# Kernel optimization log

Measured on AMD Instinct MI355X. Metric: run time of the kernel, lower is better.

The kernel has to match this reference:

```python
import jax, jax.numpy as jnp
import numpy as np

B, N, DIM = 2, 2048, 1024
HEADS, DH = 16, 64
INNER = HEADS * DH
LN_EPS = 1e-5


def setup_inputs() -> dict:
    key = jax.random.key(0)
    ks = jax.random.split(key, 3)
    x = jax.random.normal(ks[0], (B, N, DIM), dtype=jnp.float32)
    ln_w = jnp.ones((DIM,), dtype=jnp.float32)
    ln_b = jnp.zeros((DIM,), dtype=jnp.float32)
    w_qkv = jax.random.normal(ks[1], (DIM, 3 * INNER), dtype=jnp.float32) * (DIM ** -0.5)
    w_out = jax.random.normal(ks[2], (INNER, DIM), dtype=jnp.float32) * (INNER ** -0.5)
    b_out = jnp.zeros((DIM,), dtype=jnp.float32)
    return {"x": x, "ln_w": ln_w, "ln_b": ln_b, "w_qkv": w_qkv, "w_out": w_out, "b_out": b_out}


def _rope(q, k):
    # q, k: (b, h, n, d) with d even; interleaved RoPE matching the torch module.
    n, d = q.shape[-2], q.shape[-1]
    inv_freq = jnp.exp(jnp.arange(0, d, 2, dtype=jnp.float32) * (-jnp.log(jnp.float32(10000.0)) / d))
    ang = jnp.arange(n, dtype=jnp.float32)[:, None] * inv_freq[None, :]  # (n, d/2)
    cos = jnp.repeat(jnp.cos(ang), 2, axis=-1)  # (n, d) -> broadcast over b,h
    sin = jnp.repeat(jnp.sin(ang), 2, axis=-1)

    def rot(t):
        t2 = t.reshape(*t.shape[:-1], d // 2, 2)  # pairs (even, odd)
        t2 = jnp.stack([-t2[..., 1], t2[..., 0]], axis=-1).reshape(t.shape)
        return t * cos + t2 * sin

    return rot(q), rot(k)


def reference(x, ln_w, ln_b, w_qkv, w_out, b_out):
    # LayerNorm
    mu = jnp.mean(x, axis=-1, keepdims=True)
    var = jnp.var(x, axis=-1, keepdims=True)
    xn = (x - mu) * jax.lax.rsqrt(var + LN_EPS) * ln_w + ln_b
    # QKV projection (no bias)
    qkv = xn @ w_qkv  # (b, n, 3*inner)
    q, k, v = jnp.split(qkv, 3, axis=-1)
    split_heads = lambda t: t.reshape(B, N, HEADS, DH).transpose(0, 2, 1, 3)  # b h n d
    q, k, v = split_heads(q), split_heads(k), split_heads(v)
    q, k = _rope(q, k)
    scale = DH ** -0.5
    dots = jnp.einsum('bhid,bhjd->bhij', q, k) * scale
    attn = jax.nn.softmax(dots, axis=-1)
    out = jnp.einsum('bhij,bhjd->bhid', attn, v)
    out = out.transpose(0, 2, 1, 3).reshape(B, N, INNER)  # b n (h d)
    return out @ w_out + b_out
```

## Files before the change

### kernel.cpp

```cpp
#include <hip/hip_runtime.h>

typedef unsigned short u16;
typedef unsigned int   u32;
typedef __bf16 bf16x8 __attribute__((ext_vector_type(8)));
typedef __bf16 bf16x2 __attribute__((ext_vector_type(2)));
typedef float  f32x4  __attribute__((ext_vector_type(4)));

#define B_     2
#define N_     2048
#define DIM_   1024
#define HEADS_ 16
#define DH_    64
#define BH_    (B_*HEADS_)
#define ROWS_  (B_*N_)

__device__ __forceinline__ u16 f2b(float f) {
  union { __bf16 h; u16 u; } v; v.h = (__bf16)f; return v.u;
}
__device__ __forceinline__ u32 pkb(float a, float b) {
  bf16x2 t; t[0] = (__bf16)a; t[1] = (__bf16)b;
  union { bf16x2 v; u32 u; } c; c.v = t; return c.u;
}
__device__ __forceinline__ float b2f(u16 h) {
  union { u32 u; float f; } v; v.u = ((u32)h) << 16;
  return v.f;
}
__device__ __forceinline__ void gload16(const void* g, void* l) {
  __builtin_amdgcn_global_load_lds(
      (const __attribute__((address_space(1))) void*)g,
      (__attribute__((address_space(3))) void*)l, 16, 0, 0);
}
__device__ __forceinline__ f32x4 mfma16(bf16x8 a, bf16x8 b, f32x4 c) {
  return __builtin_amdgcn_mfma_f32_16x16x32_bf16(a, b, c, 0, 0, 0);
}

__global__ __launch_bounds__(256) void prep_kernel(
    const float* __restrict__ x, const float* __restrict__ lw,
    const float* __restrict__ lb, const float* __restrict__ wqkv,
    const float* __restrict__ wout, u16* __restrict__ xn,
    u16* __restrict__ wqt, u16* __restrict__ wot) {
  __shared__ float tile[32][33];
  int blk = blockIdx.x, t = threadIdx.x;
  if (blk < 4096) {
    int r = blk;
    const float4* xr = (const float4*)(x + (size_t)r * DIM_);
    float4 v = xr[t];
    float s  = v.x + v.y + v.z + v.w;
    float s2 = v.x*v.x + v.y*v.y + v.z*v.z + v.w*v.w;
    #pragma unroll
    for (int off = 32; off >= 1; off >>= 1) {
      s  += __shfl_down(s, off);
      s2 += __shfl_down(s2, off);
    }
    int w = t >> 6, lane = t & 63;
    if (lane == 0) { tile[0][w] = s; tile[1][w] = s2; }
    __syncthreads();
    if (t == 0) {
      float S = tile[0][0]+tile[0][1]+tile[0][2]+tile[0][3];
      float S2 = tile[1][0]+tile[1][1]+tile[1][2]+tile[1][3];
      float mu = S * (1.0f/DIM_);
      float var = S2 * (1.0f/DIM_) - mu*mu;
      tile[2][0] = mu; tile[2][1] = rsqrtf(var + 1e-5f);
    }
    __syncthreads();
    float mu = tile[2][0], rs = tile[2][1];
    float4 wv = ((const float4*)lw)[t];
    float4 bv = ((const float4*)lb)[t];
    u32 lo = pkb((v.x-mu)*rs*wv.x + bv.x, (v.y-mu)*rs*wv.y + bv.y);
    u32 hi = pkb((v.z-mu)*rs*wv.z + bv.z, (v.w-mu)*rs*wv.w + bv.w);
    ((uint2*)xn)[(size_t)r*256 + t] = make_uint2(lo, hi);
  } else {
    const float* in; u16* outp; int R, C, c0, r0;
    if (blk < 7168) {
      int b2 = blk - 4096;
      in = wqkv; outp = wqt; R = 1024; C = 3072;
      c0 = (b2 % 96) * 32; r0 = (b2 / 96) * 32;
    } else {
      int b2 = blk - 7168;
      in = wout; outp = wot; R = 1024; C = 1024;
      c0 = (b2 & 31) * 32; r0 = (b2 >> 5) * 32;
    }
    int tx = t & 31, ty = t >> 5;
    #pragma unroll
    for (int i = 0; i < 4; i++)
      tile[ty + i*8][tx] = in[(size_t)(r0 + ty + i*8) * C + c0 + tx];
    __syncthreads();
    #pragma unroll
    for (int i = 0; i < 4; i++)
      outp[(size_t)(c0 + ty + i*8) * R + r0 + tx] = f2b(tile[tx][ty + i*8]);
  }
}

__global__ __launch_bounds__(256) void gemm_qkv(
    const u16* __restrict__ A, const u16* __restrict__ Bt,
    u16* __restrict__ qo, u16* __restrict__ ko, u16* __restrict__ vo) {
  const int K = 1024;
  __shared__ __align__(16) u16 lA[128*32];
  __shared__ __align__(16) u16 lB[128*32];
  int tid = threadIdx.x;
  int lane = tid & 63;
  int w = tid >> 6, wm = w >> 1, wn = w & 1;
  int l15 = lane & 15, g = lane >> 4;
  int bm = blockIdx.x, bn = blockIdx.y;
  const f32x4 z = {0.f, 0.f, 0.f, 0.f};
  f32x4 acc[4][4];
  #pragma unroll
  for (int i = 0; i < 4; i++)
    #pragma unroll
    for (int j = 0; j < 4; j++)
      acc[i][j] = z;
  const u16* ag = A  + (size_t)(bm*128 + (tid>>2)) * K + (tid&3)*8;
  const u16* bg = Bt + (size_t)(bn*128 + (tid>>2)) * K + (tid&3)*8;
  u16* la = lA + tid*8;
  u16* lb = lB + tid*8;
  for (int k0 = 0; k0 < K; k0 += 32) {
    gload16(ag + k0,                la);
    gload16(ag + (size_t)64*K + k0, la + 2048);
    gload16(bg + k0,                lb);
    gload16(bg + (size_t)64*K + k0, lb + 2048);
    __syncthreads();
    bf16x8 af[4], bfr[4];
    #pragma unroll
    for (int mt = 0; mt < 4; mt++)
      af[mt] = *(const bf16x8*)(lA + (wm*64 + mt*16 + l15)*32 + g*8);
    #pragma unroll
    for (int nt = 0; nt < 4; nt++)
      bfr[nt] = *(const bf16x8*)(lB + (wn*64 + nt*16 + l15)*32 + g*8);
    __builtin_amdgcn_s_setprio(1);
    #pragma unroll
    for (int mt = 0; mt < 4; mt++)
      #pragma unroll
      for (int nt = 0; nt < 4; nt++)
        acc[mt][nt] = mfma16(af[mt], bfr[nt], acc[mt][nt]);
    __builtin_amdgcn_s_setprio(0);
    __syncthreads();
  }
  #pragma unroll
  for (int mt = 0; mt < 4; mt++) {
    #pragma unroll
    for (int nt = 0; nt < 4; nt++) {
      #pragma unroll
      for (int reg = 0; reg < 4; reg++) {
        int rr = bm*128 + wm*64 + mt*16 + g*4 + reg;
        int cc = bn*128 + wn*64 + nt*16 + l15;
        float val = acc[mt][nt][reg];
        int which = cc >> 10, inner = cc & 1023;
        int h = inner >> 6, dd = inner & 63;
        int b = rr >> 11, np = rr & 2047;
        int bh = b*HEADS_ + h;
        if (which == 0)      qo[((size_t)(bh*2048 + np))*64 + dd] = f2b(val);
        else if (which == 1) ko[((size_t)(bh*2048 + np))*64 + dd] = f2b(val);
        else                 vo[((size_t)(bh*64 + dd))*2048 + np] = f2b(val);
      }
    }
  }
}

__global__ __launch_bounds__(256) void rope_k_kernel(u16* k) {
  int tid = blockIdx.x * 256 + threadIdx.x;
  int row = tid >> 3, sub = tid & 7;
  int n = row & 2047;
  u32* kp = (u32*)(k + (size_t)row * 64 + sub * 8);
  uint4 uk = *(uint4*)kp;
  float c4[4], s4[4];
  #pragma unroll
  for (int j = 0; j < 4; j++) {
    int p = sub*4 + j;
    float freq = expf(-(2.0f * (float)p) * (9.210340371976184f / 64.0f));
    float ang = (float)n * freq;
    __sincosf(ang, &s4[j], &c4[j]);
  }
#define ROPE_K(u, c, s) { \
    float e = b2f((u16)(u)), o = b2f((u16)((u) >> 16)); \
    (u) = pkb(e*(c) - o*(s), o*(c) + e*(s)); }
  ROPE_K(uk.x, c4[0], s4[0]) ROPE_K(uk.y, c4[1], s4[1])
  ROPE_K(uk.z, c4[2], s4[2]) ROPE_K(uk.w, c4[3], s4[3])
#undef ROPE_K
  *(uint4*)kp = uk;
}

__global__ __launch_bounds__(256) void gemm_out(
    const u16* __restrict__ A, const u16* __restrict__ Bt,
    const float* __restrict__ bias, float* __restrict__ out) {
  const int K = 1024, N = 1024;
  __shared__ __align__(16) u16 lA[128*32];
  __shared__ __align__(16) u16 lB[64*32];
  int tid = threadIdx.x;
  int lane = tid & 63;
  int w = tid >> 6, wm = w >> 1, wn = w & 1;
  int l15 = lane & 15, g = lane >> 4;
  int bm = blockIdx.x, bn = blockIdx.y;
  const f32x4 z = {0.f, 0.f, 0.f, 0.f};
  f32x4 acc[4][2];
  #pragma unroll
  for (int i = 0; i < 4; i++)
    #pragma unroll
    for (int j = 0; j < 2; j++)
      acc[i][j] = z;
  const u16* ag = A  + (size_t)(bm*128 + (tid>>2)) * K + (tid&3)*8;
  const u16* bg = Bt + (size_t)(bn*64 + (tid>>2)) * K + (tid&3)*8;
  u16* la = lA + tid*8;
  u16* lb = lB + tid*8;
  for (int k0 = 0; k0 < K; k0 += 32) {
    gload16(ag + k0,                la);
    gload16(ag + (size_t)64*K + k0, la + 2048);
    gload16(bg + k0,                lb);
    __syncthreads();
    bf16x8 af[4], bfr[2];
    #pragma unroll
    for (int mt = 0; mt < 4; mt++)
      af[mt] = *(const bf16x8*)(lA + (wm*64 + mt*16 + l15)*32 + g*8);
    #pragma unroll
    for (int nt = 0; nt < 2; nt++)
      bfr[nt] = *(const bf16x8*)(lB + (wn*32 + nt*16 + l15)*32 + g*8);
    __builtin_amdgcn_s_setprio(1);
    #pragma unroll
    for (int mt = 0; mt < 4; mt++)
      #pragma unroll
      for (int nt = 0; nt < 2; nt++)
        acc[mt][nt] = mfma16(af[mt], bfr[nt], acc[mt][nt]);
    __builtin_amdgcn_s_setprio(0);
    __syncthreads();
  }
  #pragma unroll
  for (int mt = 0; mt < 4; mt++)
    #pragma unroll
    for (int nt = 0; nt < 2; nt++)
      #pragma unroll
      for (int reg = 0; reg < 4; reg++) {
        int rr = bm*128 + wm*64 + mt*16 + g*4 + reg;
        int cc = bn*64 + wn*32 + nt*16 + l15;
        out[(size_t)rr * N + cc] = acc[mt][nt][reg] + bias[cc];
      }
}

__global__ __launch_bounds__(512, 4) void flash_attn(
    const u16* __restrict__ qbf, const u16* __restrict__ kbf,
    const u16* __restrict__ vt, u16* __restrict__ aout) {
  __shared__ __align__(16) char smem[49152];
  char* lK = smem;
  char* lV = smem + 24576;
  int tid = threadIdx.x;
  int w = tid >> 6, lane = tid & 63;
  int l15 = lane & 15, g = lane >> 4;
  int p = w & 3, rho = w >> 2;
  int lin = blockIdx.x;
  int nb = (lin & 7) * 64 + (lin >> 3);
  int bh = nb >> 4, qb = nb & 15;
  const f32x4 z = {0.f, 0.f, 0.f, 0.f};
  const u16* qrow_base = qbf + ((size_t)bh*2048 + qb*128 + p*32) * 64;
  const float qs = 0.125f * 1.4426950408889634f;
  bf16x8 Qf[2][2];
  #pragma unroll
  for (int qt = 0; qt < 2; qt++) {
    int n = qb*128 + p*32 + qt*16 + l15;
    #pragma unroll
    for (int dh = 0; dh < 2; dh++) {
      union { bf16x8 v; u32 u[4]; } f;
      f.v = *(const bf16x8*)(qrow_base + (qt*16 + l15)*64 + dh*32 + g*8);
      #pragma unroll
      for (int j = 0; j < 4; j++) {
        int pidx = dh*16 + g*4 + j;
        float freq = expf(-(2.0f * (float)pidx) * (9.210340371976184f / 64.0f));
        float sn, cn;
        __sincosf((float)n * freq, &sn, &cn);
        float e = b2f((u16)f.u[j]), o = b2f((u16)(f.u[j] >> 16));
        f.u[j] = pkb((e*cn - o*sn)*qs, (o*cn + e*sn)*qs);
      }
      Qf[qt][dh] = f.v;
    }
  }
  const char* kb = (const char*)(kbf + (size_t)bh * 2048 * 64);
  const char* vb = (const char*)(vt  + (size_t)bh * 64 * 2048);
  int srow = tid >> 3;
  int soff = ((tid & 7) * 16) ^ ((srow & 7) << 4);
  int sl = srow & 31;
  int ksrc = (srow & 32) | (((sl >> 2) & 3) << 3) | (((sl >> 4) & 1) << 2) | (sl & 3);
  const int swz = (l15 & 7) << 4;

  float lp[2][2] = {{0.f, 0.f}, {0.f, 0.f}};
  f32x4 o[4][2];
  #pragma unroll
  for (int i = 0; i < 4; i++)
    #pragma unroll
    for (int j = 0; j < 2; j++)
      o[i][j] = z;

#define STAGE(t, buf) { \
    gload16(kb + (size_t)((t)*64 + ksrc) * 128 + soff, lK + (buf)*8192 + (size_t)tid*16); \
    gload16(vb + (size_t)srow * 4096 + (t)*128 + soff, lV + (buf)*8192 + (size_t)tid*16); }

  STAGE(0, 0)
  STAGE(1, 1)
  asm volatile("s_waitcnt vmcnt(2)" ::: "memory");
  __builtin_amdgcn_s_barrier();

  int cur = 0, pfb = 2;
  #pragma unroll 1
  for (int t = 0; t < 32; ++t) {
    if (t < 30) STAGE(t + 2, pfb)
    const char* Kc = lK + cur*8192;
    const char* Vc = lV + cur*8192;
    f32x4 st[2][2];
    bf16x8 ka[2][2];
    #pragma unroll
    for (int kt = 0; kt < 2; kt++)
      #pragma unroll
      for (int dh = 0; dh < 2; dh++)
        ka[kt][dh] = *(const bf16x8*)(Kc + (rho*32 + kt*16 + l15)*128
                                         + ((dh*64 + g*16) ^ swz));
    __builtin_amdgcn_s_setprio(1);
    #pragma unroll
    for (int kt = 0; kt < 2; kt++)
      #pragma unroll
      for (int qt = 0; qt < 2; qt++) {
        f32x4 a = mfma16(ka[kt][0], Qf[qt][0], z);
        st[kt][qt] = mfma16(ka[kt][1], Qf[qt][1], a);
      }
    __builtin_amdgcn_s_setprio(0);
    #pragma unroll
    for (int kt = 0; kt < 2; kt++)
      #pragma unroll
      for (int qt = 0; qt < 2; qt++)
        #pragma unroll
        for (int r = 0; r < 4; r++) {
          float pv = __builtin_amdgcn_exp2f(st[kt][qt][r]);
          st[kt][qt][r] = pv;
          lp[qt][kt] += pv;
        }
    bf16x8 vf[4];
    #pragma unroll
    for (int dt = 0; dt < 4; dt++)
      vf[dt] = *(const bf16x8*)(Vc + (dt*16 + l15)*128 + ((rho*64 + g*16) ^ swz));
    __builtin_amdgcn_s_setprio(1);
    #pragma unroll
    for (int qt = 0; qt < 2; qt++) {
      union { u32 u[4]; bf16x8 v; } pf;
      pf.u[0] = pkb(st[0][qt][0], st[0][qt][1]);
      pf.u[1] = pkb(st[0][qt][2], st[0][qt][3]);
      pf.u[2] = pkb(st[1][qt][0], st[1][qt][1]);
      pf.u[3] = pkb(st[1][qt][2], st[1][qt][3]);
      #pragma unroll
      for (int dt = 0; dt < 4; dt++)
        o[dt][qt] = mfma16(vf[dt], pf.v, o[dt][qt]);
    }
    __builtin_amdgcn_s_setprio(0);
    if (t < 31) {
      if (t < 30) { asm volatile("s_waitcnt vmcnt(2)" ::: "memory"); }
      else        { asm volatile("s_waitcnt vmcnt(0)" ::: "memory"); }
      __builtin_amdgcn_s_barrier();
    }
    cur = (cur + 1 == 3) ? 0 : cur + 1;
    pfb = (pfb + 1 == 3) ? 0 : pfb + 1;
  }
#undef STAGE

  float ls[2];
  #pragma unroll
  for (int qt = 0; qt < 2; qt++) {
    ls[qt] = lp[qt][0] + lp[qt][1];
    ls[qt] += __shfl_xor(ls[qt], 16);
    ls[qt] += __shfl_xor(ls[qt], 32);
  }
  __syncthreads();

  float* lspx = (float*)(smem + 32768);
  if (rho == 1) {
    #pragma unroll
    for (int dt = 0; dt < 4; dt++)
      #pragma unroll
      for (int qt = 0; qt < 2; qt++) {
        int ql = qt*16 + l15;
        int off = p*8192 + ql*256 + ((dt*64 + g*16) ^ ((ql & 7) << 4));
        *(f32x4*)(smem + off) = o[dt][qt];
      }
    if (g == 0) {
      lspx[p*64 + l15]      = ls[0];
      lspx[p*64 + 16 + l15] = ls[1];
    }
  }
  __syncthreads();
  float rls[2] = {0.f, 0.f};
  if (rho == 0) {
    #pragma unroll
    for (int qt = 0; qt < 2; qt++)
      rls[qt] = 1.0f / (ls[qt] + lspx[p*64 + qt*16 + l15]);
    #pragma unroll
    for (int dt = 0; dt < 4; dt++)
      #pragma unroll
      for (int qt = 0; qt < 2; qt++) {
        int ql = qt*16 + l15;
        int off = p*8192 + ql*256 + ((dt*64 + g*16) ^ ((ql & 7) << 4));
        o[dt][qt] += *(const f32x4*)(smem + off);
      }
  }
  __syncthreads();
  if (rho == 0) {
    #pragma unroll
    for (int dt = 0; dt < 4; dt++)
      #pragma unroll
      for (int qt = 0; qt < 2; qt++) {
        int ql = qt*16 + l15;
        u32 w0 = pkb(o[dt][qt][0]*rls[qt], o[dt][qt][1]*rls[qt]);
        u32 w1 = pkb(o[dt][qt][2]*rls[qt], o[dt][qt][3]*rls[qt]);
        int d2 = dt*32 + g*8;
        *(uint2*)(smem + p*8192 + ql*128 + (d2 ^ ((ql & 7) << 4))) =
            make_uint2(w0, w1);
      }
  }
  __syncthreads();
  int row = tid >> 2;
  int b = bh >> 4, h = bh & 15;
  int n = qb*128 + row;
  #pragma unroll
  for (int j = 0; j < 2; j++) {
    int slot = (tid & 3)*2 + j;
    uint4 rv = *(const uint4*)(smem + (row >> 5)*8192 + (row & 31)*128
                               + ((slot*16) ^ ((row & 7) << 4)));
    *(uint4*)(aout + ((size_t)(b*2048 + n))*1024 + h*64 + slot*8) = rv;
  }
}

extern "C" void kernel_launch(void* const* d_in, const int* in_sizes, int n_in,
                              void* d_out, int out_size, void* d_ws, size_t ws_size,
                              hipStream_t stream) {
  const float* x    = (const float*)d_in[0];
  const float* lw   = (const float*)d_in[1];
  const float* lb   = (const float*)d_in[2];
  const float* wqkv = (const float*)d_in[3];
  const float* wout = (const float*)d_in[4];
  const float* bout = (const float*)d_in[5];
  float* out = (float*)d_out;

  char* ws = (char*)d_ws;
  size_t off = 0;
  auto alloc = [&](size_t bytes) {
    char* p = ws + off;
    off += (bytes + 255) & ~(size_t)255;
    return p;
  };
  u16* xn   = (u16*)alloc((size_t)ROWS_*DIM_*2);
  u16* wqt  = (u16*)alloc((size_t)3072*1024*2);
  u16* wot  = (u16*)alloc((size_t)1024*1024*2);
  u16* qb   = (u16*)alloc((size_t)BH_*2048*64*2);
  u16* kb   = (u16*)alloc((size_t)BH_*2048*64*2);
  u16* vtb  = (u16*)alloc((size_t)BH_*2048*64*2);
  u16* aout = (u16*)alloc((size_t)ROWS_*1024*2);

  prep_kernel<<<8192, 256, 0, stream>>>(x, lw, lb, wqkv, wout, xn, wqt, wot);
  gemm_qkv<<<dim3(32, 24), 256, 0, stream>>>(xn, wqt, qb, kb, vtb);
  rope_k_kernel<<<2048, 256, 0, stream>>>(kb);
  flash_attn<<<512, 512, 0, stream>>>(qb, kb, vtb, aout);
  gemm_out<<<dim3(32, 16), 256, 0, stream>>>(aout, wot, bout, out);
}
```

Measured before the change: 115.0 us.

## Unroll attention loop by three and compute softmax denominators via MFMA

The flash-attention main loop is unrolled by three so the triple-buffer indices and prefetch targets become compile-time constants, and the LDS address offsets are precomputed once outside the loop. The per-element VALU accumulation of softmax row sums, along with the cross-lane shuffle reduction afterward, is replaced by an extra MFMA per query tile that multiplies the bf16 probabilities by a ones vector. This moves VALU adds onto the matrix unit and removes per-iteration index arithmetic. The cost is a larger code footprint, extra MFMA work, and denominators summed from bf16-rounded probabilities instead of fp32 ones.

```diff
diff --git a/kernel.cpp b/kernel.cpp
--- a/kernel.cpp
+++ b/kernel.cpp
@@ -238,8 +238,6 @@
     const u16* __restrict__ qbf, const u16* __restrict__ kbf,
     const u16* __restrict__ vt, u16* __restrict__ aout) {
   __shared__ __align__(16) char smem[49152];
-  char* lK = smem;
-  char* lV = smem + 24576;
   int tid = threadIdx.x;
   int w = tid >> 6, lane = tid & 63;
   int l15 = lane & 15, g = lane >> 4;
@@ -278,7 +276,25 @@
   int ksrc = (srow & 32) | (((sl >> 2) & 3) << 3) | (((sl >> 4) & 1) << 2) | (sl & 3);
   const int swz = (l15 & 7) << 4;
 
-  float lp[2][2] = {{0.f, 0.f}, {0.f, 0.f}};
+  const size_t kgo = (size_t)ksrc * 128 + soff;
+  const size_t vgo = (size_t)srow * 4096 + soff;
+  const int ldk = tid * 16;
+  const int ldv = 24576 + tid * 16;
+  int koff[2][2], voff[4];
+  #pragma unroll
+  for (int kt = 0; kt < 2; kt++)
+    #pragma unroll
+    for (int dh = 0; dh < 2; dh++)
+      koff[kt][dh] = (rho*32 + kt*16 + l15)*128 + ((dh*64 + g*16) ^ swz);
+  #pragma unroll
+  for (int dt = 0; dt < 4; dt++)
+    voff[dt] = 24576 + (dt*16 + l15)*128 + ((rho*64 + g*16) ^ swz);
+
+  bf16x8 ones;
+  #pragma unroll
+  for (int i = 0; i < 8; i++) ones[i] = (__bf16)1.0f;
+
+  f32x4 den[2] = {z, z};
   f32x4 o[4][2];
   #pragma unroll
   for (int i = 0; i < 4; i++)
@@ -286,82 +302,78 @@
     for (int j = 0; j < 2; j++)
       o[i][j] = z;
 
-#define STAGE(t, buf) { \
-    gload16(kb + (size_t)((t)*64 + ksrc) * 128 + soff, lK + (buf)*8192 + (size_t)tid*16); \
-    gload16(vb + (size_t)srow * 4096 + (t)*128 + soff, lV + (buf)*8192 + (size_t)tid*16); }
+#define STAGE(T, BUF) { \
+    gload16(kb + (size_t)(T)*8192 + kgo, smem + (BUF)*8192 + ldk); \
+    gload16(vb + (size_t)(T)*128  + vgo, smem + (BUF)*8192 + ldv); }
+
+#define FBODY(T, CUR, PFB, DOSTAGE, WM) { \
+    if (DOSTAGE) STAGE((T) + 2, PFB) \
+    f32x4 st[2][2]; \
+    bf16x8 ka[2][2]; \
+    _Pragma("unroll") \
+    for (int kt = 0; kt < 2; kt++) \
+      _Pragma("unroll") \
+      for (int dh = 0; dh < 2; dh++) \
+        ka[kt][dh] = *(const bf16x8*)(smem + (CUR)*8192 + koff[kt][dh]); \
+    __builtin_amdgcn_s_setprio(1); \
+    _Pragma("unroll") \
+    for (int kt = 0; kt < 2; kt++) \
+      _Pragma("unroll") \
+      for (int qt = 0; qt < 2; qt++) { \
+        f32x4 a = mfma16(ka[kt][0], Qf[qt][0], z); \
+        st[kt][qt] = mfma16(ka[kt][1], Qf[qt][1], a); \
+      } \
+    __builtin_amdgcn_s_setprio(0); \
+    _Pragma("unroll") \
+    for (int kt = 0; kt < 2; kt++) \
+      _Pragma("unroll") \
+      for (int qt = 0; qt < 2; qt++) \
+        _Pragma("unroll") \
+        for (int r = 0; r < 4; r++) \
+          st[kt][qt][r] = __builtin_amdgcn_exp2f(st[kt][qt][r]); \
+    bf16x8 vf[4]; \
+    _Pragma("unroll") \
+    for (int dt = 0; dt < 4; dt++) \
+      vf[dt] = *(const bf16x8*)(smem + (CUR)*8192 + voff[dt]); \
+    __builtin_amdgcn_s_setprio(1); \
+    _Pragma("unroll") \
+    for (int qt = 0; qt < 2; qt++) { \
+      union { u32 u[4]; bf16x8 v; } pf; \
+      pf.u[0] = pkb(st[0][qt][0], st[0][qt][1]); \
+      pf.u[1] = pkb(st[0][qt][2], st[0][qt][3]); \
+      pf.u[2] = pkb(st[1][qt][0], st[1][qt][1]); \
+      pf.u[3] = pkb(st[1][qt][2], st[1][qt][3]); \
+      den[qt] = mfma16(ones, pf.v, den[qt]); \
+      _Pragma("unroll") \
+      for (int dt = 0; dt < 4; dt++) \
+        o[dt][qt] = mfma16(vf[dt], pf.v, o[dt][qt]); \
+    } \
+    __builtin_amdgcn_s_setprio(0); \
+    if ((WM) == 2) { \
+      asm volatile("s_waitcnt vmcnt(2)" ::: "memory"); \
+      __builtin_amdgcn_s_barrier(); \
+    } else if ((WM) == 0) { \
+      asm volatile("s_waitcnt vmcnt(0)" ::: "memory"); \
+      __builtin_amdgcn_s_barrier(); \
+    } }
 
   STAGE(0, 0)
   STAGE(1, 1)
   asm volatile("s_waitcnt vmcnt(2)" ::: "memory");
   __builtin_amdgcn_s_barrier();
 
-  int cur = 0, pfb = 2;
   #pragma unroll 1
-  for (int t = 0; t < 32; ++t) {
-    if (t < 30) STAGE(t + 2, pfb)
-    const char* Kc = lK + cur*8192;
-    const char* Vc = lV + cur*8192;
-    f32x4 st[2][2];
-    bf16x8 ka[2][2];
-    #pragma unroll
-    for (int kt = 0; kt < 2; kt++)
-      #pragma unroll
-      for (int dh = 0; dh < 2; dh++)
-        ka[kt][dh] = *(const bf16x8*)(Kc + (rho*32 + kt*16 + l15)*128
-                                         + ((dh*64 + g*16) ^ swz));
-    __builtin_amdgcn_s_setprio(1);
-    #pragma unroll
-    for (int kt = 0; kt < 2; kt++)
-      #pragma unroll
-      for (int qt = 0; qt < 2; qt++) {
-        f32x4 a = mfma16(ka[kt][0], Qf[qt][0], z);
-        st[kt][qt] = mfma16(ka[kt][1], Qf[qt][1], a);
-      }
-    __builtin_amdgcn_s_setprio(0);
-    #pragma unroll
-    for (int kt = 0; kt < 2; kt++)
-      #pragma unroll
-      for (int qt = 0; qt < 2; qt++)
-        #pragma unroll
-        for (int r = 0; r < 4; r++) {
-          float pv = __builtin_amdgcn_exp2f(st[kt][qt][r]);
-          st[kt][qt][r] = pv;
-          lp[qt][kt] += pv;
-        }
-    bf16x8 vf[4];
-    #pragma unroll
-    for (int dt = 0; dt < 4; dt++)
-      vf[dt] = *(const bf16x8*)(Vc + (dt*16 + l15)*128 + ((rho*64 + g*16) ^ swz));
-    __builtin_amdgcn_s_setprio(1);
-    #pragma unroll
-    for (int qt = 0; qt < 2; qt++) {
-      union { u32 u[4]; bf16x8 v; } pf;
-      pf.u[0] = pkb(st[0][qt][0], st[0][qt][1]);
-      pf.u[1] = pkb(st[0][qt][2], st[0][qt][3]);
-      pf.u[2] = pkb(st[1][qt][0], st[1][qt][1]);
-      pf.u[3] = pkb(st[1][qt][2], st[1][qt][3]);
-      #pragma unroll
-      for (int dt = 0; dt < 4; dt++)
-        o[dt][qt] = mfma16(vf[dt], pf.v, o[dt][qt]);
-    }
-    __builtin_amdgcn_s_setprio(0);
-    if (t < 31) {
-      if (t < 30) { asm volatile("s_waitcnt vmcnt(2)" ::: "memory"); }
-      else        { asm volatile("s_waitcnt vmcnt(0)" ::: "memory"); }
-      __builtin_amdgcn_s_barrier();
-    }
-    cur = (cur + 1 == 3) ? 0 : cur + 1;
-    pfb = (pfb + 1 == 3) ? 0 : pfb + 1;
-  }
+  for (int tb = 0; tb < 30; tb += 3) {
+    FBODY(tb + 0, 0, 2, 1, 2)
+    FBODY(tb + 1, 1, 0, 1, 2)
+    FBODY(tb + 2, 2, 1, 1, 2)
+  }
+  FBODY(30, 0, 0, 0, 0)
+  FBODY(31, 1, 0, 0, 3)
 #undef STAGE
-
-  float ls[2];
-  #pragma unroll
-  for (int qt = 0; qt < 2; qt++) {
-    ls[qt] = lp[qt][0] + lp[qt][1];
-    ls[qt] += __shfl_xor(ls[qt], 16);
-    ls[qt] += __shfl_xor(ls[qt], 32);
-  }
+#undef FBODY
+
+  float ls[2] = {den[0][0], den[1][0]};
   __syncthreads();
 
   float* lspx = (float*)(smem + 32768);
```

Measured after the change: 111.9 us. 1.03x faster.
